# Kernel optimization log

Hardware: AMD Instinct MI355X
Metric: run time of the kernel (lower is better)

Reference implementation:

```python
import jax, jax.numpy as jnp
import numpy as np

B, S, D_MODEL, D_K, D_V, H = 2, 2048, 1024, 1024, 1024, 16


def setup_inputs() -> dict:
    key = jax.random.key(0)
    ks = jax.random.split(key, 12)
    s = 0.02
    inp = {
        "queries": jax.random.normal(ks[0], (B, S, D_MODEL), jnp.float32),
        "keys": jax.random.normal(ks[1], (B, S, D_MODEL), jnp.float32),
        "values": jax.random.normal(ks[2], (B, S, D_MODEL), jnp.float32),
        # causal mask: 1 where attention is disallowed (added as -1e9*mask)
        "mask": jnp.triu(jnp.ones((1, 1, S, S), jnp.float32), k=1),
        "Wq": jax.random.normal(ks[3], (D_MODEL, D_K), jnp.float32) * s,
        "bq": jnp.zeros((D_K,), jnp.float32),
        "Wk": jax.random.normal(ks[4], (D_MODEL, D_K), jnp.float32) * s,
        "bk": jnp.zeros((D_K,), jnp.float32),
        "Wv": jax.random.normal(ks[5], (D_MODEL, D_V), jnp.float32) * s,
        "bv": jnp.zeros((D_V,), jnp.float32),
        "Wo": jax.random.normal(ks[6], (D_K, D_MODEL), jnp.float32) * s,
        "bo": jnp.zeros((D_MODEL,), jnp.float32),
    }
    return inp


def _split_heads(x):  # [B,S,D] -> [B,H,S,D/H]
    b, s, d = x.shape
    return x.reshape(b, s, H, d // H).transpose(0, 2, 1, 3)


def reference(queries, keys, values, mask, Wq, bq, Wk, bk, Wv, bv, Wo, bo):
    q = _split_heads(queries @ Wq + bq)   # [B,H,S,hd]
    k = _split_heads(keys @ Wk + bk)
    v = _split_heads(values @ Wv + bv)
    # NOTE: original scales by sqrt(full d_k), not per-head dim (faithful quirk)
    scores = jnp.einsum("bhqd,bhkd->bhqk", q, k) / jnp.sqrt(jnp.float32(D_K))
    scores = scores + (-1e9) * mask
    w = jax.nn.softmax(scores, axis=-1)
    out = jnp.einsum("bhqk,bhkd->bhqd", w, v)        # [B,H,S,hd]
    out = out.transpose(0, 2, 1, 3).reshape(q.shape[0], q.shape[2], D_K)
    return out @ Wo + bo
```

## Files before the change

kernel.cpp:

```cpp
#include <hip/hip_runtime.h>
#include <hip/hip_bf16.h>
#include <cstdint>

typedef __bf16 bf16;
typedef __bf16 bf16x2 __attribute__((ext_vector_type(2)));
typedef __bf16 bf16x4 __attribute__((ext_vector_type(4)));
typedef __bf16 bf16x8 __attribute__((ext_vector_type(8)));
typedef float f32x4 __attribute__((ext_vector_type(4)));
typedef float f32x16 __attribute__((ext_vector_type(16)));
typedef unsigned int u32;

#define B_ 2
#define S_ 2048
#define DM 1024
#define H_ 16
#define HD 64

__device__ __forceinline__ void gload_lds16(const bf16* g, bf16* l) {
  __builtin_amdgcn_global_load_lds((const __attribute__((address_space(1))) void*)g,
                                   (__attribute__((address_space(3))) void*)l,
                                   16, 0, 0);
}

__device__ __forceinline__ u32 cvt_pk_bf16(float lo, float hi) {
  u32 r;
  asm("v_cvt_pk_bf16_f32 %0, %1, %2" : "=v"(r) : "v"(lo), "v"(hi));
  return r;
}

__global__ __launch_bounds__(256) void convert_k(const float* __restrict__ s0,
                                                 const float* __restrict__ s1,
                                                 const float* __restrict__ s2,
                                                 bf16* __restrict__ d0,
                                                 bf16* __restrict__ d1,
                                                 bf16* __restrict__ d2) {
  const float* s = (blockIdx.z == 0) ? s0 : (blockIdx.z == 1) ? s1 : s2;
  bf16* d = (blockIdx.z == 0) ? d0 : (blockIdx.z == 1) ? d1 : d2;
  const size_t i = ((size_t)blockIdx.x * 256 + threadIdx.x) * 8;
  f32x4 a = *(const f32x4*)(s + i);
  f32x4 b = *(const f32x4*)(s + i + 4);
  bf16x8 o;
#pragma unroll
  for (int j = 0; j < 4; j++) { o[j] = (bf16)a[j]; o[j + 4] = (bf16)b[j]; }
  *(bf16x8*)(d + i) = o;
}

__global__ __launch_bounds__(256) void transposeW_k(
    const float* __restrict__ w0, const float* __restrict__ w1,
    const float* __restrict__ w2, const float* __restrict__ w3,
    bf16* __restrict__ t0, bf16* __restrict__ t1,
    bf16* __restrict__ t2, bf16* __restrict__ t3) {
  const float* src = (blockIdx.z == 0) ? w0 : (blockIdx.z == 1) ? w1
                     : (blockIdx.z == 2) ? w2 : w3;
  bf16* dst = (blockIdx.z == 0) ? t0 : (blockIdx.z == 1) ? t1
              : (blockIdx.z == 2) ? t2 : t3;
  __shared__ float tile[32][33];
  const int tx = threadIdx.x, ty = threadIdx.y;
  const int x0 = blockIdx.x * 32, y0 = blockIdx.y * 32;
#pragma unroll
  for (int r = 0; r < 4; r++)
    tile[ty + r * 8][tx] = src[(size_t)(y0 + ty + r * 8) * DM + x0 + tx];
  __syncthreads();
#pragma unroll
  for (int r = 0; r < 4; r++)
    dst[(size_t)(x0 + ty + r * 8) * DM + y0 + tx] = (bf16)tile[tx][ty + r * 8];
}

struct GArgs { const void* A; const bf16* Bt; const float* bias; void* C; };
struct GArgs3 { GArgs g[3]; };

__global__ __launch_bounds__(512, 2) void gemm256_k(GArgs3 args, int M, int N,
                                                    int K, int tilesY, int tilesX) {
  const int nwg = gridDim.x;
  const int id = blockIdx.x;
  const int wgid = (id & 7) * (nwg >> 3) + (id >> 3);
  const int perz = tilesY * tilesX;
  const int z = wgid / perz;
  const int rem = wgid - z * perz;
  const int ty = rem / tilesX, tx = rem - (rem / tilesX) * tilesX;
  const GArgs ga = args.g[z];
  const int m0 = ty * 256, n0 = tx * 256;

  __shared__ __align__(16) bf16 As[2][16384];
  __shared__ __align__(16) bf16 Bs[2][16384];

  const int tid = threadIdx.x;
  const int lane = tid & 63, w = tid >> 6;
  const int l15 = lane & 15, q = lane >> 4;
  const int wr = w >> 2, wc = w & 3;

  const bf16* gA[4];
  const bf16* gB[4];
#pragma unroll
  for (int i = 0; i < 4; i++) {
    const int ci = i * 512 + w * 64 + lane;
    const int row = ci >> 3, ch = ci & 7, sc = ch ^ (row & 7);
    gA[i] = (const bf16*)ga.A + (size_t)(m0 + row) * K + sc * 8;
    gB[i] = ga.Bt + (size_t)(n0 + row) * K + sc * 8;
  }

  const int cA0 = ((q) ^ (l15 & 7)) * 8;
  const int cA1 = ((4 + q) ^ (l15 & 7)) * 8;

  f32x4 acc[8][4] = {};

#pragma unroll
  for (int i = 0; i < 4; i++) {
    gload_lds16(gA[i], &As[0][(i * 512 + w * 64) * 8]);
    gload_lds16(gB[i], &Bs[0][(i * 512 + w * 64) * 8]);
  }
  asm volatile("s_waitcnt vmcnt(0)" ::: "memory");
  __builtin_amdgcn_s_barrier();

  const int NT = K >> 6;
  for (int t = 0; t < NT; ++t) {
    const int cur = t & 1;
    const bf16* Ac = As[cur];
    const bf16* Bc = Bs[cur];

    bf16x8 a[4][2], b[2][2][2];
#pragma unroll
    for (int mt = 0; mt < 4; mt++) {
      const int row = wr * 128 + mt * 16 + l15;
      a[mt][0] = *(const bf16x8*)(Ac + row * 64 + cA0);
      a[mt][1] = *(const bf16x8*)(Ac + row * 64 + cA1);
    }
#pragma unroll
    for (int nt = 0; nt < 2; nt++) {
      const int row = wc * 64 + nt * 16 + l15;
      b[0][nt][0] = *(const bf16x8*)(Bc + row * 64 + cA0);
      b[0][nt][1] = *(const bf16x8*)(Bc + row * 64 + cA1);
    }
    if (t + 1 < NT) {
      const int k0 = (t + 1) << 6;
      bf16* An = As[cur ^ 1];
      bf16* Bn = Bs[cur ^ 1];
#pragma unroll
      for (int i = 0; i < 4; i++) {
        gload_lds16(gA[i] + k0, An + (i * 512 + w * 64) * 8);
        gload_lds16(gB[i] + k0, Bn + (i * 512 + w * 64) * 8);
      }
    }
    __builtin_amdgcn_s_setprio(1);
#pragma unroll
    for (int mt = 0; mt < 4; mt++)
#pragma unroll
      for (int nt = 0; nt < 2; nt++)
#pragma unroll
        for (int kk = 0; kk < 2; kk++)
          acc[mt][nt] = __builtin_amdgcn_mfma_f32_16x16x32_bf16(
              a[mt][kk], b[0][nt][kk], acc[mt][nt], 0, 0, 0);
    __builtin_amdgcn_s_setprio(0);
    __builtin_amdgcn_s_barrier();

#pragma unroll
    for (int nt = 0; nt < 2; nt++) {
      const int row = wc * 64 + 32 + nt * 16 + l15;
      b[1][nt][0] = *(const bf16x8*)(Bc + row * 64 + cA0);
      b[1][nt][1] = *(const bf16x8*)(Bc + row * 64 + cA1);
    }
    __builtin_amdgcn_s_setprio(1);
#pragma unroll
    for (int mt = 0; mt < 4; mt++)
#pragma unroll
      for (int nt = 0; nt < 2; nt++)
#pragma unroll
        for (int kk = 0; kk < 2; kk++)
          acc[mt][2 + nt] = __builtin_amdgcn_mfma_f32_16x16x32_bf16(
              a[mt][kk], b[1][nt][kk], acc[mt][2 + nt], 0, 0, 0);
    __builtin_amdgcn_s_setprio(0);
    __builtin_amdgcn_s_barrier();

#pragma unroll
    for (int mt = 0; mt < 4; mt++) {
      const int row = wr * 128 + 64 + mt * 16 + l15;
      a[mt][0] = *(const bf16x8*)(Ac + row * 64 + cA0);
      a[mt][1] = *(const bf16x8*)(Ac + row * 64 + cA1);
    }
    __builtin_amdgcn_s_setprio(1);
#pragma unroll
    for (int mt = 0; mt < 4; mt++)
#pragma unroll
      for (int nt = 0; nt < 2; nt++)
#pragma unroll
        for (int kk = 0; kk < 2; kk++)
          acc[4 + mt][2 + nt] = __builtin_amdgcn_mfma_f32_16x16x32_bf16(
              a[mt][kk], b[1][nt][kk], acc[4 + mt][2 + nt], 0, 0, 0);
    __builtin_amdgcn_s_setprio(0);
    __builtin_amdgcn_s_barrier();

    __builtin_amdgcn_s_setprio(1);
#pragma unroll
    for (int mt = 0; mt < 4; mt++)
#pragma unroll
      for (int nt = 0; nt < 2; nt++)
#pragma unroll
        for (int kk = 0; kk < 2; kk++)
          acc[4 + mt][nt] = __builtin_amdgcn_mfma_f32_16x16x32_bf16(
              a[mt][kk], b[0][nt][kk], acc[4 + mt][nt], 0, 0, 0);
    __builtin_amdgcn_s_setprio(0);
    asm volatile("s_waitcnt vmcnt(0)" ::: "memory");
    __builtin_amdgcn_s_barrier();
  }

#pragma unroll
  for (int nh = 0; nh < 2; nh++)
#pragma unroll
    for (int nt = 0; nt < 2; nt++) {
      const int col = n0 + wc * 64 + nh * 32 + nt * 16 + l15;
      const float bv = ga.bias[col];
#pragma unroll
      for (int mh = 0; mh < 2; mh++)
#pragma unroll
        for (int mt = 0; mt < 4; mt++) {
          const int row = m0 + wr * 128 + mh * 64 + mt * 16 + q * 4;
          f32x4 v = acc[mh * 4 + mt][nh * 2 + nt];
#pragma unroll
          for (int r = 0; r < 4; r++)
            ((bf16*)ga.C)[(size_t)(row + r) * N + col] = (bf16)(v[r] + bv);
        }
    }
}

template <bool AF32, bool CF32>
__global__ __launch_bounds__(256) void gemm_k(GArgs3 args, int M, int N, int K) {
  const GArgs ga = args.g[blockIdx.z];
  __shared__ __align__(16) bf16 As[128 * 32];
  __shared__ __align__(16) bf16 Bs[128 * 32];
  const int tid = threadIdx.x;
  const int lane = tid & 63, w = tid >> 6;
  const int l15 = lane & 15, q = lane >> 4;
  const int wr = w >> 1, wc = w & 1;

  int bx = blockIdx.x, by = blockIdx.y;
  if constexpr (CF32) {
    const int nb = gridDim.x * gridDim.y;
    const int id = by * gridDim.x + bx;
    const int wg = (id & 7) * (nb >> 3) + (id >> 3);
    bx = wg % gridDim.x;
    by = wg / gridDim.x;
  }
  const int m0 = by * 128, n0 = bx * 128;

  const int c0 = w * 128 + lane;
  const int c1 = c0 + 64;
  const int r0 = c0 >> 2, r1 = c1 >> 2, koff = (c0 & 3) * 8;
  const bf16* gB0 = ga.Bt + (size_t)(n0 + r0) * K + koff;
  const bf16* gB1 = ga.Bt + (size_t)(n0 + r1) * K + koff;
  bf16* lA0 = As + (w * 2 + 0) * 512;
  bf16* lA1 = As + (w * 2 + 1) * 512;
  bf16* lB0 = Bs + (w * 2 + 0) * 512;
  bf16* lB1 = Bs + (w * 2 + 1) * 512;

  const float* pA0 = nullptr;
  const float* pA1 = nullptr;
  f32x4 t00, t01, t10, t11;
  if constexpr (AF32) {
    const float* A = (const float*)ga.A;
    pA0 = A + (size_t)(m0 + r0) * K + koff;
    pA1 = A + (size_t)(m0 + r1) * K + koff;
    t00 = *(const f32x4*)pA0; t01 = *(const f32x4*)(pA0 + 4);
    t10 = *(const f32x4*)pA1; t11 = *(const f32x4*)(pA1 + 4);
  }

  f32x4 acc[4][4] = {};

  for (int k0 = 0; k0 < K; k0 += 32) {
    if constexpr (AF32) {
      bf16x8 va0, va1;
#pragma unroll
      for (int j = 0; j < 4; j++) {
        va0[j] = (bf16)t00[j]; va0[j + 4] = (bf16)t01[j];
        va1[j] = (bf16)t10[j]; va1[j + 4] = (bf16)t11[j];
      }
      *(bf16x8*)(lA0 + lane * 8) = va0;
      *(bf16x8*)(lA1 + lane * 8) = va1;
    } else {
      const bf16* A = (const bf16*)ga.A;
      gload_lds16(A + (size_t)(m0 + r0) * K + koff + k0, lA0);
      gload_lds16(A + (size_t)(m0 + r1) * K + koff + k0, lA1);
    }
    gload_lds16(gB0 + k0, lB0);
    gload_lds16(gB1 + k0, lB1);
    __syncthreads();

    bf16x8 a[4], b[4];
#pragma unroll
    for (int mt = 0; mt < 4; mt++)
      a[mt] = *(const bf16x8*)(As + (wr * 64 + mt * 16 + l15) * 32 + q * 8);
#pragma unroll
    for (int nt = 0; nt < 4; nt++)
      b[nt] = *(const bf16x8*)(Bs + (wc * 64 + nt * 16 + l15) * 32 + q * 8);

    if constexpr (AF32) {
      const int kn = (k0 + 32 < K) ? k0 + 32 : k0;
      t00 = *(const f32x4*)(pA0 + kn); t01 = *(const f32x4*)(pA0 + kn + 4);
      t10 = *(const f32x4*)(pA1 + kn); t11 = *(const f32x4*)(pA1 + kn + 4);
    }

#pragma unroll
    for (int mt = 0; mt < 4; mt++)
#pragma unroll
      for (int nt = 0; nt < 4; nt++)
        acc[mt][nt] = __builtin_amdgcn_mfma_f32_16x16x32_bf16(a[mt], b[nt],
                                                              acc[mt][nt], 0, 0, 0);
    __syncthreads();
  }

#pragma unroll
  for (int nt = 0; nt < 4; nt++) {
    const int col = n0 + wc * 64 + nt * 16 + l15;
    const float bv = ga.bias[col];
#pragma unroll
    for (int mt = 0; mt < 4; mt++) {
      const int row = m0 + wr * 64 + mt * 16 + q * 4;
#pragma unroll
      for (int r = 0; r < 4; r++) {
        const float val = acc[mt][nt][r] + bv;
        if constexpr (CF32)
          ((float*)ga.C)[(size_t)(row + r) * N + col] = val;
        else
          ((bf16*)ga.C)[(size_t)(row + r) * N + col] = (bf16)val;
      }
    }
  }
}

__global__ __launch_bounds__(256, 4) void attn_k(const bf16* __restrict__ Qp,
                                                 const bf16* __restrict__ Kp,
                                                 const bf16* __restrict__ Vp,
                                                 bf16* __restrict__ Op) {
  const int g = blockIdx.x;
  const int c = g & 255, sl = g >> 8;
  const int u = c & 31;
  const int xt = (sl == 0) ? u : (sl == 1) ? 31 - u
                 : (sl == 2) ? (u ^ 16) : 31 - (u ^ 16);
  const int h = (c >> 5) | ((sl & 1) << 3);
  const int b = sl >> 1;
  const int i0 = xt * 64;

  const int tid = threadIdx.x;
  const int lane = tid & 63, w = tid >> 6;
  const int l31 = lane & 31, hi = lane >> 5;
  const int qh = w >> 1, kh = w & 1;

  __shared__ __align__(16) char smem[36864];
  bf16 (*Ks)[64][72] = (bf16 (*)[64][72])smem;
  bf16 (*Vts)[64][72] = (bf16 (*)[64][72])(smem + 18432);

  const size_t headoff = (size_t)b * S_ * DM + h * HD;
  const bf16* Kb = Kp + headoff;
  const bf16* Vb = Vp + headoff;

  const int kr0 = tid >> 3, kr1 = 32 + (tid >> 3), kcb = (tid & 7) * 8;
  const int d0 = (tid & 31) * 2, kq = (tid >> 5) * 8;
  const float QSCALE = 0.04508422f;

  bf16x8 qreg[4];
  {
    const bf16* qb = Qp + headoff + (size_t)(i0 + qh * 32 + l31) * DM + hi * 8;
#pragma unroll
    for (int kk = 0; kk < 4; kk++) {
      bf16x8 v = *(const bf16x8*)(qb + kk * 16);
      bf16x8 o;
#pragma unroll
      for (int j = 0; j < 8; j++) o[j] = (bf16)((float)v[j] * QSCALE);
      qreg[kk] = o;
    }
  }

  {
    bf16x8 k0v = *(const bf16x8*)(Kb + (size_t)kr0 * DM + kcb);
    bf16x8 k1v = *(const bf16x8*)(Kb + (size_t)kr1 * DM + kcb);
    *(bf16x8*)&Ks[0][kr0][kcb] = k0v;
    *(bf16x8*)&Ks[0][kr1][kcb] = k1v;
    bf16x8 vlo, vhi;
#pragma unroll
    for (int j = 0; j < 8; j++) {
      bf16x2 p = *(const bf16x2*)(Vb + (size_t)(kq + j) * DM + d0);
      vlo[j] = p[0]; vhi[j] = p[1];
    }
    *(bf16x8*)&Vts[0][d0][kq] = vlo;
    *(bf16x8*)&Vts[0][d0 + 1][kq] = vhi;
  }
  __syncthreads();

  f32x16 oacc0 = {}, oacc1 = {};
  float rsum = 0.f;
  int buf = 0;

  for (int j0 = 0; j0 <= i0; j0 += 64, buf ^= 1) {
    const int jn = (j0 + 64 <= i0) ? j0 + 64 : 0;
    bf16x8 kpre0 = *(const bf16x8*)(Kb + (size_t)(jn + kr0) * DM + kcb);
    bf16x8 kpre1 = *(const bf16x8*)(Kb + (size_t)(jn + kr1) * DM + kcb);
    bf16x2 vpre[8];
#pragma unroll
    for (int j = 0; j < 8; j++)
      vpre[j] = *(const bf16x2*)(Vb + (size_t)(jn + kq + j) * DM + d0);

    const bool diag = (j0 == i0);
    if (!(diag && kh > qh)) {
      f32x16 sacc = {};
      __builtin_amdgcn_s_setprio(1);
#pragma unroll
      for (int kk = 0; kk < 4; kk++) {
        bf16x8 ka = *(const bf16x8*)&Ks[buf][kh * 32 + l31][kk * 16 + hi * 8];
        sacc = __builtin_amdgcn_mfma_f32_32x32x16_bf16(ka, qreg[kk], sacc, 0, 0, 0);
      }
      __builtin_amdgcn_s_setprio(0);

      float p[16];
      if (diag) {
        const int qrl = qh * 32 + l31;
#pragma unroll
        for (int r = 0; r < 16; r++) {
          const int keyl = kh * 32 + (r & 3) + 8 * (r >> 2) + 4 * hi;
          p[r] = (keyl <= qrl) ? __builtin_amdgcn_exp2f(sacc[r]) : 0.f;
          rsum += p[r];
        }
      } else {
#pragma unroll
        for (int r = 0; r < 16; r++) {
          p[r] = __builtin_amdgcn_exp2f(sacc[r]);
          rsum += p[r];
        }
      }

      u32 Aq[4][2];
#pragma unroll
      for (int t = 0; t < 4; t++) {
        Aq[t][0] = cvt_pk_bf16(p[4 * t + 0], p[4 * t + 1]);
        Aq[t][1] = cvt_pk_bf16(p[4 * t + 2], p[4 * t + 3]);
      }
      bf16x8 pb[2];
#pragma unroll
      for (int s = 0; s < 2; s++) {
        auto e0 = __builtin_amdgcn_permlane32_swap(Aq[2 * s][0], Aq[2 * s + 1][0], false, false);
        auto e1 = __builtin_amdgcn_permlane32_swap(Aq[2 * s][1], Aq[2 * s + 1][1], false, false);
        union { u32 u[4]; bf16x8 v; } cv;
        cv.u[0] = e0[0]; cv.u[1] = e1[0]; cv.u[2] = e0[1]; cv.u[3] = e1[1];
        pb[s] = cv.v;
      }

      __builtin_amdgcn_s_setprio(1);
#pragma unroll
      for (int s = 0; s < 2; s++) {
        bf16x8 va0 = *(const bf16x8*)&Vts[buf][l31][kh * 32 + s * 16 + hi * 8];
        bf16x8 va1 = *(const bf16x8*)&Vts[buf][32 + l31][kh * 32 + s * 16 + hi * 8];
        oacc0 = __builtin_amdgcn_mfma_f32_32x32x16_bf16(va0, pb[s], oacc0, 0, 0, 0);
        oacc1 = __builtin_amdgcn_mfma_f32_32x32x16_bf16(va1, pb[s], oacc1, 0, 0, 0);
      }
      __builtin_amdgcn_s_setprio(0);
    }

    *(bf16x8*)&Ks[buf ^ 1][kr0][kcb] = kpre0;
    *(bf16x8*)&Ks[buf ^ 1][kr1][kcb] = kpre1;
    {
      bf16x8 vlo, vhi;
#pragma unroll
      for (int j = 0; j < 8; j++) { vlo[j] = vpre[j][0]; vhi[j] = vpre[j][1]; }
      *(bf16x8*)&Vts[buf ^ 1][d0][kq] = vlo;
      *(bf16x8*)&Vts[buf ^ 1][d0 + 1][kq] = vhi;
    }
    __syncthreads();
  }

  float rtot_w = rsum + __shfl_xor(rsum, 32);
  float* osum = (float*)smem;
  float* auxf = (float*)(smem + 32768);
#pragma unroll
  for (int m = 0; m < 2; m++) {
#pragma unroll
    for (int rq = 0; rq < 4; rq++) {
      f32x4 v4;
#pragma unroll
      for (int e = 0; e < 4; e++)
        v4[e] = m ? oacc1[rq * 4 + e] : oacc0[rq * 4 + e];
      *(f32x4*)(osum + w * 2048 + (m * 4 + rq) * 256 + lane * 4) = v4;
    }
  }
  if (lane < 32) auxf[w * 32 + lane] = rtot_w;
  __syncthreads();

  {
    const int q = tid >> 2, q31b = q & 31, qh2 = q >> 5;
    const float rtot = auxf[(qh2 * 2 + 0) * 32 + q31b] + auxf[(qh2 * 2 + 1) * 32 + q31b];
    const float rinv = 1.0f / rtot;
    const int dbase = (tid & 3) * 16;
    bf16* orow = Op + headoff + (size_t)(i0 + q) * DM + dbase;
#pragma unroll
    for (int gg = 0; gg < 2; gg++) {
      bf16x8 o8;
#pragma unroll
      for (int e = 0; e < 8; e++) {
        const int d = dbase + gg * 8 + e;
        const int base = (((d >> 5) << 2) | ((d >> 3) & 3)) * 256 +
                         (q31b + 32 * ((d >> 2) & 1)) * 4 + (d & 3);
        const float v = osum[(qh2 * 2 + 0) * 2048 + base] +
                        osum[(qh2 * 2 + 1) * 2048 + base];
        o8[e] = (bf16)(v * rinv);
      }
      *(bf16x8*)(orow + gg * 8) = o8;
    }
  }
}

extern "C" void kernel_launch(void* const* d_in, const int* in_sizes, int n_in,
                              void* d_out, int out_size, void* d_ws, size_t ws_size,
                              hipStream_t stream) {
  const float* q_in = (const float*)d_in[0];
  const float* k_in = (const float*)d_in[1];
  const float* v_in = (const float*)d_in[2];
  const float* Wq = (const float*)d_in[4];
  const float* bq = (const float*)d_in[5];
  const float* Wk = (const float*)d_in[6];
  const float* bk = (const float*)d_in[7];
  const float* Wv = (const float*)d_in[8];
  const float* bv = (const float*)d_in[9];
  const float* Wo = (const float*)d_in[10];
  const float* bo = (const float*)d_in[11];

  bf16* ws = (bf16*)d_ws;
  const size_t NQ = (size_t)B_ * S_ * DM;
  bf16* Qp = ws;
  bf16* Kp = ws + NQ;
  bf16* Vp = ws + 2 * NQ;
  bf16* WqT = ws + 3 * NQ;
  bf16* WkT = WqT + (size_t)DM * DM;
  bf16* WvT = WkT + (size_t)DM * DM;
  bf16* WoT = WvT + (size_t)DM * DM;
  bf16* qb = WoT + (size_t)DM * DM;
  bf16* kb = qb + NQ;
  bf16* vb = kb + NQ;

  const bool fast = ws_size >= (size_t)(28 * 1024 * 1024) * 2;

  transposeW_k<<<dim3(32, 32, 4), dim3(32, 8), 0, stream>>>(
      Wq, Wk, Wv, Wo, WqT, WkT, WvT, WoT);

  if (fast) {
    convert_k<<<dim3((B_ * S_ * DM) / (256 * 8), 1, 3), 256, 0, stream>>>(
        q_in, k_in, v_in, qb, kb, vb);
    GArgs3 g3;
    g3.g[0] = {qb, WqT, bq, Qp};
    g3.g[1] = {kb, WkT, bk, Kp};
    g3.g[2] = {vb, WvT, bv, Vp};
    gemm256_k<<<dim3(192), 512, 0, stream>>>(g3, B_ * S_, DM, DM, 16, 4);
  } else {
    GArgs3 g3;
    g3.g[0] = {q_in, WqT, bq, Qp};
    g3.g[1] = {k_in, WkT, bk, Kp};
    g3.g[2] = {v_in, WvT, bv, Vp};
    gemm_k<true, false><<<dim3(DM / 128, (B_ * S_) / 128, 3), 256, 0, stream>>>(
        g3, B_ * S_, DM, DM);
  }

  attn_k<<<dim3(1024, 1, 1), 256, 0, stream>>>(Qp, Kp, Vp, Qp);

  GArgs3 gp;
  gp.g[0] = {Qp, WoT, bo, d_out};
  gp.g[1] = gp.g[0];
  gp.g[2] = gp.g[0];
  gemm_k<false, true><<<dim3(DM / 128, (B_ * S_) / 128, 1), 256, 0, stream>>>(
      gp, B_ * S_, DM, DM);
}
```

Measured before the change: 225.5 us.

## Deepen attention K/V prefetch, XOR-swizzle LDS, remap blocks per XCD

```diff
diff --git a/kernel.cpp b/kernel.cpp
--- a/kernel.cpp
+++ b/kernel.cpp
@@ -331,12 +331,13 @@
                                                  const bf16* __restrict__ Vp,
                                                  bf16* __restrict__ Op) {
   const int g = blockIdx.x;
-  const int c = g & 255, sl = g >> 8;
-  const int u = c & 31;
-  const int xt = (sl == 0) ? u : (sl == 1) ? 31 - u
-                 : (sl == 2) ? (u ^ 16) : 31 - (u ^ 16);
-  const int h = (c >> 5) | ((sl & 1) << 3);
-  const int b = sl >> 1;
+  const int xcd = g & 7, s = g >> 3;
+  const int gl = s & 3, tau = s >> 2;
+  const int bh = xcd * 4 + gl;
+  const int b = bh >> 4, h = bh & 15;
+  const int o3 = tau & 7, hq = tau >> 3;
+  const int xt = (hq == 0) ? o3 : (hq == 1) ? 15 - o3
+                 : (hq == 2) ? 16 + o3 : 31 - o3;
   const int i0 = xt * 64;
 
   const int tid = threadIdx.x;
@@ -344,16 +345,19 @@
   const int l31 = lane & 31, hi = lane >> 5;
   const int qh = w >> 1, kh = w & 1;
 
-  __shared__ __align__(16) char smem[36864];
-  bf16 (*Ks)[64][72] = (bf16 (*)[64][72])smem;
-  bf16 (*Vts)[64][72] = (bf16 (*)[64][72])(smem + 18432);
+  __shared__ __align__(16) char smem[33280];
+  bf16 (*Ks)[64][64] = (bf16 (*)[64][64])smem;
+  bf16 (*Vts)[64][64] = (bf16 (*)[64][64])(smem + 16384);
 
   const size_t headoff = (size_t)b * S_ * DM + h * HD;
   const bf16* Kb = Kp + headoff;
   const bf16* Vb = Vp + headoff;
 
   const int kr0 = tid >> 3, kr1 = 32 + (tid >> 3), kcb = (tid & 7) * 8;
+  const int cK = ((tid & 7) ^ (kr0 & 7)) * 8;
   const int d0 = (tid & 31) * 2, kq = (tid >> 5) * 8;
+  const int cV0 = ((tid >> 5) ^ (d0 & 7)) * 8;
+  const int cV1 = ((tid >> 5) ^ ((d0 + 1) & 7)) * 8;
   const float QSCALE = 0.04508422f;
 
   bf16x8 qreg[4];
@@ -369,19 +373,29 @@
     }
   }
 
+  const int NI = (i0 >> 6) + 1;
+
+  bf16x8 kR0 = *(const bf16x8*)(Kb + (size_t)kr0 * DM + kcb);
+  bf16x8 kR1 = *(const bf16x8*)(Kb + (size_t)kr1 * DM + kcb);
+  bf16x2 vR[8];
+#pragma unroll
+  for (int j = 0; j < 8; j++)
+    vR[j] = *(const bf16x2*)(Vb + (size_t)(kq + j) * DM + d0);
+  *(bf16x8*)&Ks[0][kr0][cK] = kR0;
+  *(bf16x8*)&Ks[0][kr1][cK] = kR1;
   {
-    bf16x8 k0v = *(const bf16x8*)(Kb + (size_t)kr0 * DM + kcb);
-    bf16x8 k1v = *(const bf16x8*)(Kb + (size_t)kr1 * DM + kcb);
-    *(bf16x8*)&Ks[0][kr0][kcb] = k0v;
-    *(bf16x8*)&Ks[0][kr1][kcb] = k1v;
     bf16x8 vlo, vhi;
 #pragma unroll
-    for (int j = 0; j < 8; j++) {
-      bf16x2 p = *(const bf16x2*)(Vb + (size_t)(kq + j) * DM + d0);
-      vlo[j] = p[0]; vhi[j] = p[1];
-    }
-    *(bf16x8*)&Vts[0][d0][kq] = vlo;
-    *(bf16x8*)&Vts[0][d0 + 1][kq] = vhi;
+    for (int j = 0; j < 8; j++) { vlo[j] = vR[j][0]; vhi[j] = vR[j][1]; }
+    *(bf16x8*)&Vts[0][d0][cV0] = vlo;
+    *(bf16x8*)&Vts[0][d0 + 1][cV1] = vhi;
+  }
+  if (NI > 1) {
+    kR0 = *(const bf16x8*)(Kb + (size_t)(64 + kr0) * DM + kcb);
+    kR1 = *(const bf16x8*)(Kb + (size_t)(64 + kr1) * DM + kcb);
+#pragma unroll
+    for (int j = 0; j < 8; j++)
+      vR[j] = *(const bf16x2*)(Vb + (size_t)(64 + kq + j) * DM + d0);
   }
   __syncthreads();
 
@@ -389,23 +403,40 @@
   float rsum = 0.f;
   int buf = 0;
 
-  for (int j0 = 0; j0 <= i0; j0 += 64, buf ^= 1) {
-    const int jn = (j0 + 64 <= i0) ? j0 + 64 : 0;
-    bf16x8 kpre0 = *(const bf16x8*)(Kb + (size_t)(jn + kr0) * DM + kcb);
-    bf16x8 kpre1 = *(const bf16x8*)(Kb + (size_t)(jn + kr1) * DM + kcb);
-    bf16x2 vpre[8];
-#pragma unroll
-    for (int j = 0; j < 8; j++)
-      vpre[j] = *(const bf16x2*)(Vb + (size_t)(jn + kq + j) * DM + d0);
-
-    const bool diag = (j0 == i0);
+  for (int t = 0; t < NI; ++t, buf ^= 1) {
+    if (t + 1 < NI) {
+      *(bf16x8*)&Ks[buf ^ 1][kr0][cK] = kR0;
+      *(bf16x8*)&Ks[buf ^ 1][kr1][cK] = kR1;
+      bf16x8 vlo, vhi;
+#pragma unroll
+      for (int j = 0; j < 8; j++) { vlo[j] = vR[j][0]; vhi[j] = vR[j][1]; }
+      *(bf16x8*)&Vts[buf ^ 1][d0][cV0] = vlo;
+      *(bf16x8*)&Vts[buf ^ 1][d0 + 1][cV1] = vhi;
+    }
+    if (t + 2 < NI) {
+      const size_t jn = (size_t)(t + 2) * 64;
+      kR0 = *(const bf16x8*)(Kb + (jn + kr0) * DM + kcb);
+      kR1 = *(const bf16x8*)(Kb + (jn + kr1) * DM + kcb);
+#pragma unroll
+      for (int j = 0; j < 8; j++)
+        vR[j] = *(const bf16x2*)(Vb + (jn + kq + j) * DM + d0);
+    }
+
+    const bool diag = (t == NI - 1);
     if (!(diag && kh > qh)) {
-      f32x16 sacc = {};
+      f32x16 sa = {}, sb = {};
       __builtin_amdgcn_s_setprio(1);
 #pragma unroll
-      for (int kk = 0; kk < 4; kk++) {
-        bf16x8 ka = *(const bf16x8*)&Ks[buf][kh * 32 + l31][kk * 16 + hi * 8];
-        sacc = __builtin_amdgcn_mfma_f32_32x32x16_bf16(ka, qreg[kk], sacc, 0, 0, 0);
+      for (int kk = 0; kk < 2; kk++) {
+        bf16x8 ka = *(const bf16x8*)
+            &Ks[buf][kh * 32 + l31][((2 * kk + hi) ^ (l31 & 7)) * 8];
+        sa = __builtin_amdgcn_mfma_f32_32x32x16_bf16(ka, qreg[kk], sa, 0, 0, 0);
+      }
+#pragma unroll
+      for (int kk = 2; kk < 4; kk++) {
+        bf16x8 ka = *(const bf16x8*)
+            &Ks[buf][kh * 32 + l31][((2 * kk + hi) ^ (l31 & 7)) * 8];
+        sb = __builtin_amdgcn_mfma_f32_32x32x16_bf16(ka, qreg[kk], sb, 0, 0, 0);
       }
       __builtin_amdgcn_s_setprio(0);
 
@@ -415,53 +446,49 @@
 #pragma unroll
         for (int r = 0; r < 16; r++) {
           const int keyl = kh * 32 + (r & 3) + 8 * (r >> 2) + 4 * hi;
-          p[r] = (keyl <= qrl) ? __builtin_amdgcn_exp2f(sacc[r]) : 0.f;
-          rsum += p[r];
+          p[r] = (keyl <= qrl) ? __builtin_amdgcn_exp2f(sa[r] + sb[r]) : 0.f;
         }
       } else {
 #pragma unroll
-        for (int r = 0; r < 16; r++) {
-          p[r] = __builtin_amdgcn_exp2f(sacc[r]);
-          rsum += p[r];
-        }
+        for (int r = 0; r < 16; r++)
+          p[r] = __builtin_amdgcn_exp2f(sa[r] + sb[r]);
+      }
+      {
+        float q0 = (p[0] + p[1]) + (p[2] + p[3]);
+        float q1 = (p[4] + p[5]) + (p[6] + p[7]);
+        float q2 = (p[8] + p[9]) + (p[10] + p[11]);
+        float q3 = (p[12] + p[13]) + (p[14] + p[15]);
+        rsum += (q0 + q1) + (q2 + q3);
       }
 
       u32 Aq[4][2];
 #pragma unroll
-      for (int t = 0; t < 4; t++) {
-        Aq[t][0] = cvt_pk_bf16(p[4 * t + 0], p[4 * t + 1]);
-        Aq[t][1] = cvt_pk_bf16(p[4 * t + 2], p[4 * t + 3]);
+      for (int t2 = 0; t2 < 4; t2++) {
+        Aq[t2][0] = cvt_pk_bf16(p[4 * t2 + 0], p[4 * t2 + 1]);
+        Aq[t2][1] = cvt_pk_bf16(p[4 * t2 + 2], p[4 * t2 + 3]);
       }
       bf16x8 pb[2];
 #pragma unroll
-      for (int s = 0; s < 2; s++) {
-        auto e0 = __builtin_amdgcn_permlane32_swap(Aq[2 * s][0], Aq[2 * s + 1][0], false, false);
-        auto e1 = __builtin_amdgcn_permlane32_swap(Aq[2 * s][1], Aq[2 * s + 1][1], false, false);
+      for (int s2 = 0; s2 < 2; s2++) {
+        auto e0 = __builtin_amdgcn_permlane32_swap(Aq[2 * s2][0], Aq[2 * s2 + 1][0], false, false);
+        auto e1 = __builtin_amdgcn_permlane32_swap(Aq[2 * s2][1], Aq[2 * s2 + 1][1], false, false);
         union { u32 u[4]; bf16x8 v; } cv;
         cv.u[0] = e0[0]; cv.u[1] = e1[0]; cv.u[2] = e0[1]; cv.u[3] = e1[1];
-        pb[s] = cv.v;
+        pb[s2] = cv.v;
       }
 
       __builtin_amdgcn_s_setprio(1);
 #pragma unroll
-      for (int s = 0; s < 2; s++) {
-        bf16x8 va0 = *(const bf16x8*)&Vts[buf][l31][kh * 32 + s * 16 + hi * 8];
-        bf16x8 va1 = *(const bf16x8*)&Vts[buf][32 + l31][kh * 32 + s * 16 + hi * 8];
-        oacc0 = __builtin_amdgcn_mfma_f32_32x32x16_bf16(va0, pb[s], oacc0, 0, 0, 0);
-        oacc1 = __builtin_amdgcn_mfma_f32_32x32x16_bf16(va1, pb[s], oacc1, 0, 0, 0);
+      for (int s2 = 0; s2 < 2; s2++) {
+        const int cv = ((kh * 4 + s2 * 2 + hi) ^ (l31 & 7)) * 8;
+        bf16x8 va0 = *(const bf16x8*)&Vts[buf][l31][cv];
+        bf16x8 va1 = *(const bf16x8*)&Vts[buf][32 + l31][cv];
+        oacc0 = __builtin_amdgcn_mfma_f32_32x32x16_bf16(va0, pb[s2], oacc0, 0, 0, 0);
+        oacc1 = __builtin_amdgcn_mfma_f32_32x32x16_bf16(va1, pb[s2], oacc1, 0, 0, 0);
       }
       __builtin_amdgcn_s_setprio(0);
     }
 
-    *(bf16x8*)&Ks[buf ^ 1][kr0][kcb] = kpre0;
-    *(bf16x8*)&Ks[buf ^ 1][kr1][kcb] = kpre1;
-    {
-      bf16x8 vlo, vhi;
-#pragma unroll
-      for (int j = 0; j < 8; j++) { vlo[j] = vpre[j][0]; vhi[j] = vpre[j][1]; }
-      *(bf16x8*)&Vts[buf ^ 1][d0][kq] = vlo;
-      *(bf16x8*)&Vts[buf ^ 1][d0 + 1][kq] = vhi;
-    }
     __syncthreads();
   }
 
```

After: 225.7 us. About the same (+0.1%).
